# Performance work log

Hardware: AMD Instinct MI355X
Metric: run time of the kernel (lower is better)

Reference implementation:

```python
import jax, jax.numpy as jnp
import numpy as np

B, D, I = 16384, 2048, 2048


def setup_inputs() -> dict:
    key = jax.random.key(0)
    kx, kh, kw = jax.random.split(key, 3)
    x = jax.random.normal(kx, (B, I), dtype=jnp.float32)
    h = jax.random.normal(kh, (B, D), dtype=jnp.float32)
    # input projection weight (Linear, no bias): [d_model, inpt_size]
    W_ih = jax.random.normal(kw, (D, I), dtype=jnp.float32) * 0.02
    # orthogonal-ish hidden transition (torch uses an SVD-orthogonal block),
    # well-conditioned so the inverse is exact and stable
    rng = np.random.default_rng(0)
    q, _ = np.linalg.qr(rng.standard_normal((D, D)).astype(np.float64))
    W_hh = jnp.asarray(q, dtype=jnp.float32)
    W_inv = jnp.asarray(np.linalg.inv(q), dtype=jnp.float32)  # buffer self.inv
    return {"x": x, "h": h, "W_ih": W_ih, "W_hh": W_hh, "W_inv": W_inv}


def reference(x, h, W_ih, W_hh, W_inv):
    # outs = inpt_linear(x) : [B, D]
    outs = jnp.einsum("bi,di->bd", x, W_ih)
    not_trig = outs[..., -1] >= -1.0          # [B]
    h_last = h[..., -1]                        # [B]
    m_fwd = ((h_last > 0) & not_trig)[..., None]   # forward rotation branch
    m_inv = ((h_last < 0) & not_trig)[..., None]   # inverse rotation branch
    m_pass = (~not_trig)[..., None]                # passthrough branch
    hW = h @ W_hh   # torch.matmul(h, weight_hh) (no transpose)
    hI = h @ W_inv  # torch.matmul(h, inv)
    zero = jnp.zeros((), dtype=outs.dtype)
    return (outs
            + jnp.where(m_fwd, hW, zero)
            + jnp.where(m_inv, hI, zero)
            + jnp.where(m_pass, h, zero))
```

## Files before the change

kernel.cpp:

```cpp
#include <hip/hip_runtime.h>
#include <hip/hip_bf16.h>
#include <stdint.h>

#define B_ROWS 16384
#define DIM 2048
#define BK 64
#define MAXPR 17152

typedef float f32x4 __attribute__((ext_vector_type(4)));
typedef short bf16x8 __attribute__((ext_vector_type(8)));
using u16 = unsigned short;
using u32 = unsigned int;

__device__ __forceinline__ u32 pack_bf2(float a, float b) {
  __hip_bfloat162 t = __float22bfloat162_rn(float2{a, b});
  union { __hip_bfloat162 b2; u32 u; } cv;
  cv.b2 = t;
  return cv.u;
}

__device__ __forceinline__ u16 f2bf_rne(float f) {
  union { float f; u32 u; } v;
  v.f = f;
  u32 u = v.u;
  u32 r = u + 0x7FFFu + ((u >> 16) & 1u);
  return (u16)(r >> 16);
}

__device__ __forceinline__ void gload16(const void* g, void* l) {
  __builtin_amdgcn_global_load_lds(
      (const __attribute__((address_space(1))) u32*)g,
      (__attribute__((address_space(3))) u32*)l, 16, 0, 0);
}

__global__ __launch_bounds__(256) void k_flags(
    const float* __restrict__ x, const float* __restrict__ h,
    const float* __restrict__ W_ih, int* __restrict__ flags) {
  int row = blockIdx.x * 4 + (threadIdx.x >> 6);
  int lane = threadIdx.x & 63;
  const float* xr = x + (size_t)row * DIM;
  const float* wr = W_ih + (size_t)(DIM - 1) * DIM;
  double s = 0.0;
#pragma unroll
  for (int i = 0; i < 8; ++i) {
    int idx = (i * 64 + lane) * 4;
    f32x4 xv = *(const f32x4*)(xr + idx);
    f32x4 wv = *(const f32x4*)(wr + idx);
    s += (double)xv.x * wv.x + (double)xv.y * wv.y +
         (double)xv.z * wv.z + (double)xv.w * wv.w;
  }
#pragma unroll
  for (int off = 32; off > 0; off >>= 1) s += __shfl_xor(s, off);
  if (lane == 0) {
    float hl = h[(size_t)row * DIM + (DIM - 1)];
    flags[row] = (s < -1.0) ? 2 : (hl > 0.f ? 0 : (hl < 0.f ? 1 : 3));
  }
}

__global__ __launch_bounds__(256) void k_scan(const int* __restrict__ flags,
                                              int* __restrict__ iperm,
                                              int* __restrict__ meta) {
  __shared__ int sF[257], sI[257], sP[257];
  int t = threadIdx.x;
  int cF = 0, cI = 0, cP = 0;
  for (int i = 0; i < 64; ++i) {
    int f = flags[t * 64 + i];
    cF += (f == 0); cI += (f == 1); cP += (f >= 2);
  }
  sF[t + 1] = cF; sI[t + 1] = cI; sP[t + 1] = cP;
  for (int i = t; i < MAXPR; i += 256) iperm[i] = -1;
  __syncthreads();
  if (t == 0) {
    sF[0] = sI[0] = sP[0] = 0;
    for (int i = 1; i <= 256; ++i) {
      sF[i] += sF[i - 1]; sI[i] += sI[i - 1]; sP[i] += sP[i - 1];
    }
  }
  __syncthreads();
  int totF = sF[256], totI = sI[256], totP = sP[256];
  int padF = (totF + 255) & ~255;
  int padI = (totI + 255) & ~255;
  int rowsFI = padF + padI;
  int nrows = rowsFI + totP;
  if (t == 0) {
    meta[0] = (nrows + 255) >> 8;
    meta[1] = rowsFI >> 8;
    meta[2] = rowsFI;
    meta[3] = padF;
  }
  int oF = sF[t], oI = padF + sI[t], oP = rowsFI + sP[t];
  for (int i = 0; i < 64; ++i) {
    int r = t * 64 + i;
    int f = flags[r];
    if (f == 0) iperm[oF++] = r;
    else if (f == 1) iperm[oI++] = r;
    else iperm[oP++] = r;
  }
}

__global__ __launch_bounds__(256) void k_permute(
    const float* __restrict__ x, const float* __restrict__ h,
    const int* __restrict__ iperm, const int* __restrict__ meta,
    u16* __restrict__ xP, u16* __restrict__ hP) {
  int p = blockIdx.x * 4 + (threadIdx.x >> 6);
  int lane = threadIdx.x & 63;
  int rowsFI = meta[2];
  int orig = iperm[p];
  u16* xpr = xP + (size_t)p * DIM;
  u16* hpr = hP + (size_t)p * DIM;
  bool doH = p < rowsFI;
  if (orig >= 0) {
    const float* xr = x + (size_t)orig * DIM;
    const float* hr = h + (size_t)orig * DIM;
#pragma unroll
    for (int i = 0; i < 8; ++i) {
      int idx = (i * 64 + lane) * 4;
      f32x4 xv = *(const f32x4*)(xr + idx);
      *(uint2*)(xpr + idx) = uint2{pack_bf2(xv.x, xv.y), pack_bf2(xv.z, xv.w)};
      if (doH) {
        f32x4 hv = *(const f32x4*)(hr + idx);
        *(uint2*)(hpr + idx) = uint2{pack_bf2(hv.x, hv.y), pack_bf2(hv.z, hv.w)};
      }
    }
  } else {
    uint2 z{0u, 0u};
#pragma unroll
    for (int i = 0; i < 8; ++i) {
      int idx = (i * 64 + lane) * 4;
      *(uint2*)(xpr + idx) = z;
      if (doH) *(uint2*)(hpr + idx) = z;
    }
  }
}

__global__ __launch_bounds__(256) void k_convert(const float* __restrict__ src,
                                                 u16* __restrict__ dst) {
  size_t i = ((size_t)blockIdx.x * 256 + threadIdx.x) * 4;
  f32x4 v = *(const f32x4*)(src + i);
  *(uint2*)(dst + i) = uint2{pack_bf2(v.x, v.y), pack_bf2(v.z, v.w)};
}

__global__ __launch_bounds__(256) void k_transpose(const float* __restrict__ src,
                                                   u16* __restrict__ dst) {
  __shared__ float tile[32][33];
  int k0 = blockIdx.x * 32;
  int n0 = blockIdx.y * 32;
  int tx = threadIdx.x & 31;
  int ty = threadIdx.x >> 5;
#pragma unroll
  for (int i = 0; i < 4; ++i)
    tile[ty + 8 * i][tx] = src[(size_t)(k0 + ty + 8 * i) * DIM + n0 + tx];
  __syncthreads();
#pragma unroll
  for (int i = 0; i < 4; ++i)
    dst[(size_t)(n0 + ty + 8 * i) * DIM + k0 + tx] = f2bf_rne(tile[tx][ty + 8 * i]);
}

__global__ __launch_bounds__(512, 2) void k_gemm8(
    const u16* __restrict__ xP, const u16* __restrict__ hP,
    const u16* __restrict__ Wih, const u16* __restrict__ WhhT,
    const u16* __restrict__ WinvT, const int* __restrict__ iperm,
    const int* __restrict__ flags, const int* __restrict__ meta,
    const float* __restrict__ h, float* __restrict__ out) {
  __shared__ __attribute__((aligned(128))) char smem[131072];

  int o = blockIdx.x;
  int swz = (o & 7) * 67 + (o >> 3);
  int rt = swz >> 3;
  int bcol = (swz & 7) * 256;
  int brow = rt * 256;

  int nrt = meta[0];
  int tilesFI = meta[1];
  int tilesF = meta[3] >> 8;
  if (rt >= nrt) return;
  const int NTb = (rt < tilesFI) ? 64 : 32;
  const u16* Bh = (rt < tilesF) ? WhhT : WinvT;

  int t = threadIdx.x;
  int lane = t & 63;
  int wave = t >> 6;
  int wr = wave >> 2;
  int wc = wave & 3;

  int sx16 = (((lane & 3) ^ ((lane >> 3) & 3)) << 4);
  int fA = (((lane >> 4) ^ ((lane >> 1) & 3)) << 4);
  int arowbase = wr * 128 + (lane & 15);
  int browbase = wc * 64 + (lane & 15);

  auto stage = [&](int T, int isB, int kk) {
    if (T >= NTb) T -= NTb;
    int s = T >> 5;
    int kt = T & 31;
    const u16* mat;
    int r0;
    if (isB) { mat = s ? Bh : Wih; r0 = bcol; }
    else     { mat = s ? hP : xP; r0 = brow; }
    size_t gb = (size_t)(r0 + wave * 32 + (lane >> 2)) * (DIM * 2) +
                (size_t)kt * 128 + (size_t)kk * 64 + (size_t)sx16;
    char* ldst = smem + ((T & 1) << 16) + kk * 32768 + isB * 16384 +
                 (wave * 32) * 64;
    gload16((const char*)mat + gb, ldst);
    gload16((const char*)mat + gb + (size_t)16 * (DIM * 2), ldst + 1024);
  };

  f32x4 acc[8][4] = {};
  bf16x8 aF[8], bF[4];

  stage(0, 0, 0); stage(0, 1, 0);
  stage(0, 0, 1); stage(0, 1, 1);
  stage(1, 0, 0); stage(1, 1, 0);
  asm volatile("s_waitcnt vmcnt(8)" ::: "memory");
  __builtin_amdgcn_s_barrier();

#define PHASE(KK, STT, STKK)                                                   \
  {                                                                            \
    const char* Ab_ = smem + buf + (KK) * 32768;                               \
    _Pragma("unroll") for (int m = 0; m < 4; ++m) {                            \
      aF[m] = *(const bf16x8*)(Ab_ + (arowbase + m * 16) * 64 + fA);           \
      aF[4 + m] = *(const bf16x8*)(Ab_ + (arowbase + 64 + m * 16) * 64 + fA);  \
    }                                                                          \
    _Pragma("unroll") for (int n = 0; n < 4; ++n)                              \
        bF[n] = *(const bf16x8*)(Ab_ + 16384 + (browbase + n * 16) * 64 + fA); \
    stage(STT, 0, STKK);                                                       \
    stage(STT, 1, STKK);                                                       \
    asm volatile("s_waitcnt vmcnt(8)" ::: "memory");                           \
    __builtin_amdgcn_s_barrier();                                              \
    asm volatile("s_waitcnt lgkmcnt(0)" ::: "memory");                         \
    __builtin_amdgcn_sched_barrier(0);                                         \
    __builtin_amdgcn_s_setprio(1);                                             \
    _Pragma("unroll") for (int mh = 0; mh < 2; ++mh)                           \
        _Pragma("unroll") for (int m = 0; m < 4; ++m)                          \
            _Pragma("unroll") for (int n = 0; n < 4; ++n)                      \
                acc[mh * 4 + m][n] = __builtin_amdgcn_mfma_f32_16x16x32_bf16(  \
                    aF[mh * 4 + m], bF[n], acc[mh * 4 + m][n], 0, 0, 0);       \
    __builtin_amdgcn_s_setprio(0);                                             \
  }

#pragma unroll 1
  for (int T = 0; T < NTb; ++T) {
    const int buf = (T & 1) << 16;
    PHASE(0, T + 1, 1)
    PHASE(1, T + 2, 0)
  }
#undef PHASE
  asm volatile("s_waitcnt vmcnt(0)" ::: "memory");

#pragma unroll
  for (int mi = 0; mi < 8; ++mi) {
    int pbase = brow + wr * 128 + (mi >> 2) * 64 + (mi & 3) * 16 + (lane >> 4) * 4;
#pragma unroll
    for (int j = 0; j < 4; ++j) {
      int p = pbase + j;
      int orig = iperm[p];
      if (orig >= 0) {
        bool pass = (flags[orig] == 2);
#pragma unroll
        for (int n = 0; n < 4; ++n) {
          int col = bcol + wc * 64 + n * 16 + (lane & 15);
          float v = acc[mi][n][j];
          if (pass) v += h[(size_t)orig * DIM + col];
          out[(size_t)orig * DIM + col] = v;
        }
      }
    }
  }
}

#define BM 128
#define BN 128
__global__ __launch_bounds__(256, 2) void k_gemm_fb(
    const float* __restrict__ x, const float* __restrict__ h,
    const u16* __restrict__ Wih, const u16* __restrict__ WhhT,
    const u16* __restrict__ WinvT, const int* __restrict__ flags,
    float* __restrict__ out) {
  __shared__ char smem[(BM + BN) * BK * 2];
  char* sA = smem;
  char* sB = smem + BM * BK * 2;

  int o = blockIdx.x;
  int swz = (o & 7) * ((int)gridDim.x >> 3) + (o >> 3);
  int brow = (swz >> 4) * BM;
  int bcol = (swz & 15) * BN;

  int t = threadIdx.x;
  int lane = t & 63;
  int wave = t >> 6;
  int wrow = (wave >> 1) * 64;
  int wcol = (wave & 1) * 64;

  f32x4 acc[4][4] = {};
  int sc = t & 15;
  int sr0 = t >> 4;

  int aOff[4][2], bOff[4][2];
#pragma unroll
  for (int m = 0; m < 4; ++m)
#pragma unroll
    for (int kk = 0; kk < 2; ++kk) {
      int ar = wrow + m * 16 + (lane & 15);
      aOff[m][kk] = ar * (BK * 2) + ((kk * 64 + (lane >> 4) * 16) ^ ((ar & 7) << 4));
      int br = wcol + m * 16 + (lane & 15);
      bOff[m][kk] = br * (BK * 2) + ((kk * 64 + (lane >> 4) * 16) ^ ((br & 7) << 4));
    }

#pragma unroll 1
  for (int seg = 0; seg < 3; ++seg) {
    const float* Asrc = (seg == 0) ? x : h;
    const u16* Bsrc = (seg == 0) ? Wih : (seg == 1) ? WhhT : WinvT;
    int want = seg - 1;

    float rmask[8];
#pragma unroll
    for (int i = 0; i < 8; ++i) {
      int r = sr0 + 16 * i;
      rmask[i] = (want < 0 || flags[brow + r] == want) ? 1.f : 0.f;
    }

#pragma unroll 1
    for (int k0 = 0; k0 < DIM; k0 += BK) {
      __syncthreads();
#pragma unroll
      for (int i = 0; i < 8; ++i) {
        int r = sr0 + 16 * i;
        f32x4 v = *(const f32x4*)(Asrc + (size_t)(brow + r) * DIM + k0 + sc * 4);
        float msk = rmask[i];
        int off = r * (BK * 2) + ((sc * 8) ^ ((r & 7) << 4));
        *(uint2*)(sA + off) =
            uint2{pack_bf2(v.x * msk, v.y * msk), pack_bf2(v.z * msk, v.w * msk)};
      }
#pragma unroll
      for (int i = 0; i < 4; ++i) {
        int ch = t + 256 * i;
        int r = ch >> 3;
        int c = ch & 7;
        uint4 v = *(const uint4*)(Bsrc + (size_t)(bcol + r) * DIM + k0 + c * 8);
        int off = r * (BK * 2) + ((c * 16) ^ ((r & 7) << 4));
        *(uint4*)(sB + off) = v;
      }
      __syncthreads();
      bf16x8 aF2[4][2], bF2[4][2];
#pragma unroll
      for (int m = 0; m < 4; ++m)
#pragma unroll
        for (int kk = 0; kk < 2; ++kk) {
          aF2[m][kk] = *(const bf16x8*)(sA + aOff[m][kk]);
          bF2[m][kk] = *(const bf16x8*)(sB + bOff[m][kk]);
        }
#pragma unroll
      for (int kk = 0; kk < 2; ++kk)
#pragma unroll
        for (int m = 0; m < 4; ++m)
#pragma unroll
          for (int n = 0; n < 4; ++n)
            acc[m][n] = __builtin_amdgcn_mfma_f32_16x16x32_bf16(
                aF2[m][kk], bF2[n][kk], acc[m][n], 0, 0, 0);
    }
  }

#pragma unroll
  for (int m = 0; m < 4; ++m) {
    int rbase = brow + wrow + m * 16 + (lane >> 4) * 4;
#pragma unroll
    for (int j = 0; j < 4; ++j) {
      int row = rbase + j;
      bool pass = (flags[row] == 2);
#pragma unroll
      for (int n = 0; n < 4; ++n) {
        int col = bcol + wcol + n * 16 + (lane & 15);
        float v = acc[m][n][j];
        if (pass) v += h[(size_t)row * DIM + col];
        out[(size_t)row * DIM + col] = v;
      }
    }
  }
}

extern "C" void kernel_launch(void* const* d_in, const int* in_sizes, int n_in,
                              void* d_out, int out_size, void* d_ws, size_t ws_size,
                              hipStream_t stream) {
  const float* x = (const float*)d_in[0];
  const float* h = (const float*)d_in[1];
  const float* W_ih = (const float*)d_in[2];
  const float* W_hh = (const float*)d_in[3];
  const float* W_inv = (const float*)d_in[4];
  float* out = (float*)d_out;

  char* ws = (char*)d_ws;
  int* flags = (int*)ws;
  int* meta = (int*)(ws + 65536);
  int* iperm = (int*)(ws + 65536 + 256);
  u16* WihB = (u16*)(ws + 139264);
  u16* WhhT = WihB + (size_t)DIM * DIM;
  u16* WinvT = WhhT + (size_t)DIM * DIM;
  u16* xP = WinvT + (size_t)DIM * DIM;
  u16* hP = xP + (size_t)MAXPR * DIM;
  size_t need = 139264 + 3ull * DIM * DIM * 2 + 2ull * MAXPR * DIM * 2;

  k_convert<<<(DIM * DIM / 4) / 256, 256, 0, stream>>>(W_ih, WihB);
  k_transpose<<<dim3(DIM / 32, DIM / 32), 256, 0, stream>>>(W_hh, WhhT);
  k_transpose<<<dim3(DIM / 32, DIM / 32), 256, 0, stream>>>(W_inv, WinvT);
  k_flags<<<B_ROWS / 4, 256, 0, stream>>>(x, h, W_ih, flags);

  if (ws_size >= need) {
    k_scan<<<1, 256, 0, stream>>>(flags, iperm, meta);
    k_permute<<<MAXPR / 4, 256, 0, stream>>>(x, h, iperm, meta, xP, hP);
    k_gemm8<<<67 * 8, 512, 0, stream>>>(xP, hP, WihB, WhhT, WinvT, iperm,
                                        flags, meta, h, out);
  } else {
    k_gemm_fb<<<(B_ROWS / BM) * (DIM / BN), 256, 0, stream>>>(x, h, WihB, WhhT,
                                                              WinvT, flags, out);
  }
}
```

Measured before the change: 505.1 us.

## Restructure main GEMM to 256x128 tiles with 4 waves and triple-buffered LDS

The main bf16 GEMM kernel drops from 512-thread 256x256 tiles to 256-thread 256x128 tiles, which doubles the grid. The K-loop now uses a 3-stage ring of 24KB LDS buffers with a single phase per 64-wide K step, replacing the double-buffered two-half-phase scheme. The block swizzle is removed. The goal is less LDS per block, more blocks for occupancy, and deeper prefetch, at the cost of lower arithmetic intensity per tile and more redundant reloads of A.

```diff
diff --git a/kernel.cpp b/kernel.cpp
--- a/kernel.cpp
+++ b/kernel.cpp
@@ -4,7 +4,6 @@
 
 #define B_ROWS 16384
 #define DIM 2048
-#define BK 64
 #define MAXPR 17152
 
 typedef float f32x4 __attribute__((ext_vector_type(4)));
@@ -156,99 +155,97 @@
     dst[(size_t)(n0 + ty + 8 * i) * DIM + k0 + tx] = f2bf_rne(tile[tx][ty + 8 * i]);
 }
 
-__global__ __launch_bounds__(512, 2) void k_gemm8(
+__global__ __launch_bounds__(256, 2) void k_gemm8(
     const u16* __restrict__ xP, const u16* __restrict__ hP,
     const u16* __restrict__ Wih, const u16* __restrict__ WhhT,
     const u16* __restrict__ WinvT, const int* __restrict__ iperm,
     const int* __restrict__ flags, const int* __restrict__ meta,
     const float* __restrict__ h, float* __restrict__ out) {
-  __shared__ __attribute__((aligned(128))) char smem[131072];
+  __shared__ __attribute__((aligned(128))) char smem[73728];
 
   int o = blockIdx.x;
-  int swz = (o & 7) * 67 + (o >> 3);
-  int rt = swz >> 3;
-  int bcol = (swz & 7) * 256;
+  int rt = o >> 4;
+  int bcol = (o & 15) * 128;
   int brow = rt * 256;
 
   int nrt = meta[0];
   int tilesFI = meta[1];
   int tilesF = meta[3] >> 8;
   if (rt >= nrt) return;
-  const int NTb = (rt < tilesFI) ? 64 : 32;
+  const int NTb = (rt < tilesFI) ? 128 : 64;
   const u16* Bh = (rt < tilesF) ? WhhT : WinvT;
 
   int t = threadIdx.x;
   int lane = t & 63;
   int wave = t >> 6;
-  int wr = wave >> 2;
-  int wc = wave & 3;
+  int wr = wave >> 1;
+  int wc = wave & 1;
 
   int sx16 = (((lane & 3) ^ ((lane >> 3) & 3)) << 4);
   int fA = (((lane >> 4) ^ ((lane >> 1) & 3)) << 4);
   int arowbase = wr * 128 + (lane & 15);
   int browbase = wc * 64 + (lane & 15);
 
-  auto stage = [&](int T, int isB, int kk) {
-    if (T >= NTb) T -= NTb;
-    int s = T >> 5;
-    int kt = T & 31;
-    const u16* mat;
-    int r0;
-    if (isB) { mat = s ? Bh : Wih; r0 = bcol; }
-    else     { mat = s ? hP : xP; r0 = brow; }
-    size_t gb = (size_t)(r0 + wave * 32 + (lane >> 2)) * (DIM * 2) +
-                (size_t)kt * 128 + (size_t)kk * 64 + (size_t)sx16;
-    char* ldst = smem + ((T & 1) << 16) + kk * 32768 + isB * 16384 +
-                 (wave * 32) * 64;
-    gload16((const char*)mat + gb, ldst);
-    gload16((const char*)mat + gb + (size_t)16 * (DIM * 2), ldst + 1024);
+  auto stage = [&](int dT, int p) {
+    int seg = dT >> 6;
+    int kb = (dT & 63) * 64;
+    const u16* Am = seg ? hP : xP;
+    const u16* Bm = seg ? Bh : Wih;
+    char* pb = smem + p * 24576;
+#pragma unroll
+    for (int i = 0; i < 4; ++i) {
+      int r = wave * 64 + i * 16 + (lane >> 2);
+      gload16((const char*)Am + (size_t)(brow + r) * (DIM * 2) + kb + sx16,
+              pb + wave * 4096 + i * 1024);
+    }
+#pragma unroll
+    for (int i = 0; i < 2; ++i) {
+      int r = wave * 32 + i * 16 + (lane >> 2);
+      gload16((const char*)Bm + (size_t)(bcol + r) * (DIM * 2) + kb + sx16,
+              pb + 16384 + wave * 2048 + i * 1024);
+    }
   };
 
   f32x4 acc[8][4] = {};
   bf16x8 aF[8], bF[4];
 
-  stage(0, 0, 0); stage(0, 1, 0);
-  stage(0, 0, 1); stage(0, 1, 1);
-  stage(1, 0, 0); stage(1, 1, 0);
-  asm volatile("s_waitcnt vmcnt(8)" ::: "memory");
+  stage(0, 0);
+  stage(1, 1);
+  asm volatile("s_waitcnt vmcnt(6)" ::: "memory");
   __builtin_amdgcn_s_barrier();
 
-#define PHASE(KK, STT, STKK)                                                   \
-  {                                                                            \
-    const char* Ab_ = smem + buf + (KK) * 32768;                               \
-    _Pragma("unroll") for (int m = 0; m < 4; ++m) {                            \
-      aF[m] = *(const bf16x8*)(Ab_ + (arowbase + m * 16) * 64 + fA);           \
-      aF[4 + m] = *(const bf16x8*)(Ab_ + (arowbase + 64 + m * 16) * 64 + fA);  \
-    }                                                                          \
-    _Pragma("unroll") for (int n = 0; n < 4; ++n)                              \
-        bF[n] = *(const bf16x8*)(Ab_ + 16384 + (browbase + n * 16) * 64 + fA); \
-    stage(STT, 0, STKK);                                                       \
-    stage(STT, 1, STKK);                                                       \
-    asm volatile("s_waitcnt vmcnt(8)" ::: "memory");                           \
-    __builtin_amdgcn_s_barrier();                                              \
-    asm volatile("s_waitcnt lgkmcnt(0)" ::: "memory");                         \
-    __builtin_amdgcn_sched_barrier(0);                                         \
-    __builtin_amdgcn_s_setprio(1);                                             \
-    _Pragma("unroll") for (int mh = 0; mh < 2; ++mh)                           \
-        _Pragma("unroll") for (int m = 0; m < 4; ++m)                          \
-            _Pragma("unroll") for (int n = 0; n < 4; ++n)                      \
-                acc[mh * 4 + m][n] = __builtin_amdgcn_mfma_f32_16x16x32_bf16(  \
-                    aF[mh * 4 + m], bF[n], acc[mh * 4 + m][n], 0, 0, 0);       \
-    __builtin_amdgcn_s_setprio(0);                                             \
-  }
-
+  int pcur = 0;
 #pragma unroll 1
   for (int T = 0; T < NTb; ++T) {
-    const int buf = (T & 1) << 16;
-    PHASE(0, T + 1, 1)
-    PHASE(1, T + 2, 0)
-  }
-#undef PHASE
+    int pst = pcur + 2; if (pst >= 3) pst -= 3;
+    int nx = T + 2; if (nx >= NTb) nx -= NTb;
+    stage(nx, pst);
+    const char* pb = smem + pcur * 24576;
+#pragma unroll
+    for (int m = 0; m < 8; ++m)
+      aF[m] = *(const bf16x8*)(pb + (arowbase + m * 16) * 64 + fA);
+#pragma unroll
+    for (int n = 0; n < 4; ++n)
+      bF[n] = *(const bf16x8*)(pb + 16384 + (browbase + n * 16) * 64 + fA);
+    asm volatile("s_waitcnt lgkmcnt(0)" ::: "memory");
+    __builtin_amdgcn_sched_barrier(0);
+    asm volatile("s_waitcnt vmcnt(6)" ::: "memory");
+    __builtin_amdgcn_s_barrier();
+    __builtin_amdgcn_s_setprio(1);
+#pragma unroll
+    for (int m = 0; m < 8; ++m)
+#pragma unroll
+      for (int n = 0; n < 4; ++n)
+        acc[m][n] = __builtin_amdgcn_mfma_f32_16x16x32_bf16(
+            aF[m], bF[n], acc[m][n], 0, 0, 0);
+    __builtin_amdgcn_s_setprio(0);
+    pcur = (pcur == 2) ? 0 : pcur + 1;
+  }
   asm volatile("s_waitcnt vmcnt(0)" ::: "memory");
 
 #pragma unroll
   for (int mi = 0; mi < 8; ++mi) {
-    int pbase = brow + wr * 128 + (mi >> 2) * 64 + (mi & 3) * 16 + (lane >> 4) * 4;
+    int pbase = brow + wr * 128 + mi * 16 + (lane >> 4) * 4;
 #pragma unroll
     for (int j = 0; j < 4; ++j) {
       int p = pbase + j;
@@ -269,6 +266,7 @@
 
 #define BM 128
 #define BN 128
+#define BK 64
 __global__ __launch_bounds__(256, 2) void k_gemm_fb(
     const float* __restrict__ x, const float* __restrict__ h,
     const u16* __restrict__ Wih, const u16* __restrict__ WhhT,
@@ -405,8 +403,8 @@
   if (ws_size >= need) {
     k_scan<<<1, 256, 0, stream>>>(flags, iperm, meta);
     k_permute<<<MAXPR / 4, 256, 0, stream>>>(x, h, iperm, meta, xP, hP);
-    k_gemm8<<<67 * 8, 512, 0, stream>>>(xP, hP, WihB, WhhT, WinvT, iperm,
-                                        flags, meta, h, out);
+    k_gemm8<<<67 * 16, 256, 0, stream>>>(xP, hP, WihB, WhhT, WinvT, iperm,
+                                         flags, meta, h, out);
   } else {
     k_gemm_fb<<<(B_ROWS / BM) * (DIM / BN), 256, 0, stream>>>(x, h, WihB, WhhT,
                                                               WinvT, flags, out);
```

New measurement: 512.9 us. About the same (+1.5%).
